# Kernel optimization log

Hardware: AMD Instinct MI355X
Metric: run time of the kernel (lower is better)

Reference implementation:

```python
import jax, jax.numpy as jnp
import numpy as np

B, S, D_IN, D_OUT = 8, 4096, 512, 64

def setup_inputs() -> dict:
    key = jax.random.key(0)
    k1, k2, k3, k4 = jax.random.split(key, 4)
    scale = 1.0 / np.sqrt(D_IN)
    return {
        "x": jax.random.normal(k1, (B, S, D_IN), dtype=jnp.float32),
        "W_Q": jax.random.normal(k2, (D_IN, D_OUT), dtype=jnp.float32) * scale,
        "W_K": jax.random.normal(k3, (D_IN, D_OUT), dtype=jnp.float32) * scale,
        "W_V": jax.random.normal(k4, (D_IN, D_OUT), dtype=jnp.float32) * scale,
    }

def reference(x, W_Q, W_K, W_V):
    # q,k,v: [B,S,D_OUT]
    q = jnp.einsum("bsd,de->bse", x, W_Q)
    k = jnp.einsum("bsd,de->bse", x, W_K)
    v = jnp.einsum("bsd,de->bse", x, W_V)
    d_out = k.shape[-1]
    # scores: [B,S,S], causal mask (upper triangle -> -inf)
    scores = jnp.einsum("bqe,bke->bqk", q, k)
    s = q.shape[1]
    causal = jnp.tril(jnp.ones((s, s), dtype=bool))
    scores = jnp.where(causal[None, :, :], scores, -jnp.inf)
    attn = jax.nn.softmax(scores / jnp.sqrt(jnp.asarray(d_out, scores.dtype)), axis=-1)
    # dropout p=0.0 (eval) -> identity
    return jnp.einsum("bqk,bke->bqe", attn, v)
```

## Files before the change

kernel.cpp:

```cpp
#include <hip/hip_runtime.h>
#include <hip/hip_bf16.h>

#define B_    8
#define S_    4096
#define DIN   512
#define DOUT  64
#define NROWS (B_ * S_)

typedef __attribute__((ext_vector_type(8)))  short bf16x8;
typedef __attribute__((ext_vector_type(4)))  float f32x4;
typedef __attribute__((ext_vector_type(16))) float f32x16;
typedef __attribute__((ext_vector_type(2)))  unsigned int u32x2;
typedef __attribute__((ext_vector_type(2)))  int i32x2;

typedef const __attribute__((address_space(1))) unsigned int GUI;
typedef __attribute__((address_space(3))) unsigned int LUI;

__device__ __forceinline__ unsigned short f32_to_bf16(float f) {
    union { float f; unsigned int u; } c; c.f = f;
    unsigned int r = (c.u + 0x7FFFu + ((c.u >> 16) & 1u)) >> 16;
    return (unsigned short)r;
}
__device__ __forceinline__ float bf16_to_f32(unsigned short us) {
    union { unsigned int u; float f; } c; c.u = (unsigned int)us << 16;
    return c.f;
}

__device__ __forceinline__ float fast_exp2(float x) {
#if __has_builtin(__builtin_amdgcn_exp2f)
    return __builtin_amdgcn_exp2f(x);
#else
    return exp2f(x);
#endif
}

__device__ __forceinline__ float sum_xor32(float v) {
    i32x2 r = __builtin_amdgcn_permlane32_swap(__float_as_int(v), __float_as_int(v),
                                               false, false);
    return __int_as_float(r.x) + __int_as_float(r.y);
}

#define LDS_READS_DONE_FENCE() do {                                   \
    asm volatile("s_waitcnt lgkmcnt(0)" ::: "memory");                \
    __builtin_amdgcn_sched_barrier(0);                                \
} while (0)

__device__ __forceinline__ int pidx_of(int tp, int j) {
    if (tp < 16) return tp - 8;
    if (tp < 24) return 8 + (tp - 16) * 2 + (j - 1);
    return 24 + (tp - 24) * 3 + (j - 1);
}

#define PART_STRIDE 16896

__global__ void wt_convert(const float* __restrict__ WQ,
                           const float* __restrict__ WK,
                           const float* __restrict__ WV,
                           unsigned short* __restrict__ Wt2) {
    int idx = blockIdx.x * 256 + threadIdx.x;
    if (idx >= 3 * 512 * 16) return;
    int p   = idx / 8192;
    int rem = idx - p * 8192;
    int k   = rem >> 4;
    int n0  = (rem & 15) * 4;
    const float* W = (p == 0) ? WQ : ((p == 1) ? WK : WV);
    float4 v = *(const float4*)(W + k * 64 + n0);
    const int ks = k >> 5, kl = k & 31;
    float vv[4] = {v.x, v.y, v.z, v.w};
#pragma unroll
    for (int r = 0; r < 4; ++r) {
        int n = n0 + r;
        Wt2[(size_t)((ks * 12 + p * 4 + (n >> 4)) * 512) + (n & 15) * 32 + kl] =
            f32_to_bf16(vv[r]);
    }
}

__global__ __launch_bounds__(256) void qkv_proj(const float* __restrict__ x,
                                                const unsigned short* __restrict__ Wt2,
                                                unsigned short* __restrict__ QKV) {
    __shared__ alignas(16) float          xtile[2][1024];
    __shared__ alignas(16) unsigned short btile[2][6144];

    const int tid  = threadIdx.x;
    const int lane = tid & 63;
    const int wq   = tid >> 6;
    const int c15  = lane & 15;
    const int g    = lane >> 4;
    const float* xblk = x + (size_t)blockIdx.x * 32 * DIN;

    const int rw     = (wq & 1) * 16 + c15;
    const int nfbase = (wq >> 1) * 6;

    const int xrow = wq * 8 + (lane >> 3);
    const int xsl  = (lane & 7) ^ (xrow & 7);

    auto stage = [&](int slot, int ks) {
        __builtin_amdgcn_global_load_lds((GUI*)(xblk + ks * 32 + xrow * DIN + xsl * 4),
                                         (LUI*)((char*)&xtile[slot][0] + wq * 1024), 16, 0, 0);
        const unsigned short* Bs = Wt2 + (size_t)ks * 6144;
#pragma unroll
        for (int j = 0; j < 3; ++j)
            __builtin_amdgcn_global_load_lds((GUI*)(Bs + (j * 256 + tid) * 8),
                                             (LUI*)((char*)&btile[slot][0] + j * 4096 + wq * 1024),
                                             16, 0, 0);
    };
    stage(0, 0);
    stage(1, 1);

    f32x4 acc[6] = {};

    int cur = 0;
    for (int ks = 0; ks < 16; ++ks) {
        asm volatile("s_waitcnt vmcnt(4)" ::: "memory");
        asm volatile("s_barrier" ::: "memory");

        const char* xb = (const char*)&xtile[cur][0] + rw * 128;
        f32x4 a0 = *(const f32x4*)(xb + (((2 * g)     ^ (rw & 7)) << 4));
        f32x4 a1 = *(const f32x4*)(xb + (((2 * g + 1) ^ (rw & 7)) << 4));
        union { unsigned w[4]; bf16x8 v; } af;
        asm("v_cvt_pk_bf16_f32 %0, %1, %2" : "=v"(af.w[0]) : "v"(a0[0]), "v"(a0[1]));
        asm("v_cvt_pk_bf16_f32 %0, %1, %2" : "=v"(af.w[1]) : "v"(a0[2]), "v"(a0[3]));
        asm("v_cvt_pk_bf16_f32 %0, %1, %2" : "=v"(af.w[2]) : "v"(a1[0]), "v"(a1[1]));
        asm("v_cvt_pk_bf16_f32 %0, %1, %2" : "=v"(af.w[3]) : "v"(a1[2]), "v"(a1[3]));

        const char* bb = (const char*)&btile[cur][0] + c15 * 64 + g * 16;
#pragma unroll
        for (int n = 0; n < 6; ++n) {
            bf16x8 bf = *(const bf16x8*)(bb + (nfbase + n) * 1024);
            acc[n] = __builtin_amdgcn_mfma_f32_16x16x32_bf16(af.v, bf, acc[n], 0, 0, 0);
        }

        LDS_READS_DONE_FENCE();
        asm volatile("s_barrier" ::: "memory");
        {
            int tn = ks + 2; if (tn > 15) tn = 15;
            stage(cur, tn);
        }
        cur ^= 1;
    }
    asm volatile("s_waitcnt vmcnt(0)" ::: "memory");

    const int orow0 = blockIdx.x * 32 + (wq & 1) * 16 + g * 4;
#pragma unroll
    for (int n = 0; n < 6; ++n) {
        const int nfg  = nfbase + n;
        const int p    = nfg >> 2;
        const int ncol = (nfg & 3) * 16 + c15;
        if (p < 2) {
            unsigned short* outp = QKV + (size_t)p * NROWS * DOUT;
            const float sc = (p == 0) ? 0.125f * 1.44269504089f : 1.0f;
#pragma unroll
            for (int r = 0; r < 4; ++r)
                outp[(size_t)(orow0 + r) * DOUT + ncol] = f32_to_bf16(acc[n][r] * sc);
        } else {
            const int bb2  = orow0 >> 12;
            const int srow = orow0 & 4095;
            union { unsigned short s[4]; u32x2 d; } pk;
#pragma unroll
            for (int r = 0; r < 4; ++r) pk.s[r] = f32_to_bf16(acc[n][r]);
            *(u32x2*)(QKV + (size_t)2 * NROWS * DOUT +
                      ((size_t)bb2 * DOUT + ncol) * S_ + srow) = pk.d;
        }
    }
}

__global__ __launch_bounds__(512) void qk_norms(const unsigned short* __restrict__ QKV,
                                                float* __restrict__ qn,
                                                float* __restrict__ ktm) {
    __shared__ float lds[64];
    const int bid  = blockIdx.x;
    const bool isK = bid >= 512;
    const int blk  = isK ? bid - 512 : bid;
    const int tid  = threadIdx.x;
    const int rowl = tid >> 3;
    const int part = tid & 7;
    const size_t row = (size_t)blk * 64 + rowl;

    const unsigned short* src = QKV + (isK ? (size_t)NROWS * DOUT : 0) +
                                row * DOUT + part * 8;
    bf16x8 v = *(const bf16x8*)src;
    float s = 0.f;
#pragma unroll
    for (int i2 = 0; i2 < 8; ++i2) {
        float f = bf16_to_f32((unsigned short)v[i2]);
        s += f * f;
    }
    s += __shfl_xor(s, 1, 64);
    s += __shfl_xor(s, 2, 64);
    s += __shfl_xor(s, 4, 64);

    if (!isK) {
        if (part == 0) qn[row] = sqrtf(s);
    } else {
        if (part == 0) lds[rowl] = s;
        __syncthreads();
        if (tid < 64) {
            float m = lds[tid];
#pragma unroll
            for (int st = 32; st >= 1; st >>= 1)
                m = fmaxf(m, __shfl_xor(m, st, 64));
            if (tid == 0) ktm[blk] = sqrtf(m);
        }
    }
}

__global__ void kpref(const float* __restrict__ ktm, float* __restrict__ pm) {
    const int b = threadIdx.x;
    if (b >= 8) return;
    float m = 0.f;
    for (int t = 0; t < 64; ++t) {
        m = fmaxf(m, ktm[b * 64 + t]);
        pm[b * 64 + t] = m;
    }
}

__global__ __launch_bounds__(256) void attn_fwd(const unsigned short* __restrict__ QKV,
                                                const float* __restrict__ qn,
                                                const float* __restrict__ pm,
                                                float* __restrict__ out,
                                                char* __restrict__ part1,
                                                float* __restrict__ ml0) {
    __shared__ alignas(16) unsigned short k_lds[2][4096];
    __shared__ alignas(16) unsigned short v_lds[2][4096];

    const int bid = blockIdx.x;
    const int b   = bid & 7;
    const int i   = 79 - (bid >> 3);
    int tp, j;
    if      (i < 8)  { tp = i;                   j = 0; }
    else if (i < 24) { tp = 8 + ((i - 8) >> 1);  j = (i - 8) & 1; }
    else if (i < 48) { tp = 16 + (i - 24) / 3;   j = (i - 24) % 3; }
    else             { tp = 24 + ((i - 48) >> 2); j = (i - 48) & 3; }
    const int qb       = tp * 128;
    const int tile_lo  = 16 * j;
    const int tile_hi  = min(16 * j + 15, 2 * tp + 1);
    const int tile_cnt = tile_hi - tile_lo + 1;

    const int tid  = threadIdx.x;
    const int lane = tid & 63;
    const int wq   = tid >> 6;
    const int q31  = lane & 31;
    const int h    = lane >> 5;
    const int swz  = q31 & 7;
    const int rb0  = q31 * 128;

    const unsigned short* Qg  = QKV + (size_t)b * S_ * DOUT;
    const unsigned short* Kg  = QKV + (size_t)NROWS * DOUT + (size_t)b * S_ * DOUT;
    const unsigned short* VTg = QKV + (size_t)2 * NROWS * DOUT + (size_t)b * DOUT * S_;

    const int qrow = qb + wq * 32 + q31;
    const unsigned short* Qr = Qg + (size_t)qrow * DOUT + 8 * h;
    bf16x8 qf[4];
#pragma unroll
    for (int s = 0; s < 4; ++s) qf[s] = *(const bf16x8*)(Qr + 16 * s);

    const float M_r = qn[(size_t)b * S_ + qrow] * pm[b * 64 + (qrow >> 6)];
    asm volatile("s_waitcnt vmcnt(0)" ::: "memory");

    const int i0 = wq * 128 + lane;
    const int i1 = i0 + 64;
    const int r0 = i0 >> 3, s0g = (i0 & 7) ^ (r0 & 7);
    const int r1 = i1 >> 3, s1g = (i1 & 7) ^ (r1 & 7);

    auto stage = [&](int slot, int tg) {
        const unsigned short* Kt = Kg + (size_t)tg * 64 * DOUT;
        const unsigned short* Vt = VTg + tg * 64;
        char* kbase = (char*)&k_lds[slot][0] + wq * 2048;
        char* vbase = (char*)&v_lds[slot][0] + wq * 2048;
        __builtin_amdgcn_global_load_lds((GUI*)(Kt + r0 * DOUT + s0g * 8), (LUI*)kbase, 16, 0, 0);
        __builtin_amdgcn_global_load_lds((GUI*)(Kt + r1 * DOUT + s1g * 8), (LUI*)(kbase + 1024), 16, 0, 0);
        __builtin_amdgcn_global_load_lds((GUI*)(Vt + (size_t)r0 * S_ + s0g * 8), (LUI*)vbase, 16, 0, 0);
        __builtin_amdgcn_global_load_lds((GUI*)(Vt + (size_t)r1 * S_ + s1g * 8), (LUI*)(vbase + 1024), 16, 0, 0);
    };

    stage(0, tile_lo);
    stage(1, tile_lo + 1);

    f32x16 oacc0 = {}, oacc1 = {};
    float l_r = 0.f;

    int cur = 0;
    for (int itl = 0; itl < tile_cnt; ++itl) {
        const int tg = tile_lo + itl;
        asm volatile("s_waitcnt vmcnt(4)" ::: "memory");
        asm volatile("s_barrier" ::: "memory");

        const char* kb_ = (const char*)&k_lds[cur][0];
        const char* vb_ = (const char*)&v_lds[cur][0];

        f32x16 sA = {}, sB = {};
#pragma unroll
        for (int s = 0; s < 4; ++s) {
            const int sl = ((2 * s + h) ^ swz) << 4;
            bf16x8 ka  = *(const bf16x8*)(kb_ + rb0 + sl);
            bf16x8 kb2 = *(const bf16x8*)(kb_ + rb0 + 4096 + sl);
            sA = __builtin_amdgcn_mfma_f32_32x32x16_bf16(ka,  qf[s], sA, 0, 0, 0);
            sB = __builtin_amdgcn_mfma_f32_32x32x16_bf16(kb2, qf[s], sB, 0, 0, 0);
        }

        if (tg >= 2 * tp) {
#pragma unroll
            for (int r2 = 0; r2 < 16; ++r2) {
                const int kvg = 64 * tg + (r2 & 3) + 8 * (r2 >> 2) + 4 * h;
                if (kvg      > qrow) sA[r2] = -1.0e30f;
                if (kvg + 32 > qrow) sB[r2] = -1.0e30f;
            }
        }

        float t0 = 0.f, t1 = 0.f, t2 = 0.f, t3 = 0.f;
#pragma unroll
        for (int k2 = 0; k2 < 16; ++k2) {
            sA[k2] = fast_exp2(sA[k2] - M_r);
            sB[k2] = fast_exp2(sB[k2] - M_r);
        }
#pragma unroll
        for (int k2 = 0; k2 < 4; ++k2) {
            t0 += sA[k2];      t1 += sA[k2 + 4];
            t0 += sA[k2 + 8];  t1 += sA[k2 + 12];
            t2 += sB[k2];      t3 += sB[k2 + 4];
            t2 += sB[k2 + 8];  t3 += sB[k2 + 12];
        }
        l_r += (t0 + t1) + (t2 + t3);

#define STEP_PV(u, Pv) do {                                                        \
        const int e0 = 2 * ((u) & 1);                                              \
        unsigned pa, pb2, pc, pd;                                                  \
        asm("v_cvt_pk_bf16_f32 %0, %1, %2" : "=v"(pa)  : "v"(Pv[4*e0+0]), "v"(Pv[4*e0+1])); \
        asm("v_cvt_pk_bf16_f32 %0, %1, %2" : "=v"(pb2) : "v"(Pv[4*e0+2]), "v"(Pv[4*e0+3])); \
        asm("v_cvt_pk_bf16_f32 %0, %1, %2" : "=v"(pc)  : "v"(Pv[4*e0+4]), "v"(Pv[4*e0+5])); \
        asm("v_cvt_pk_bf16_f32 %0, %1, %2" : "=v"(pd)  : "v"(Pv[4*e0+6]), "v"(Pv[4*e0+7])); \
        i32x2 ra = __builtin_amdgcn_permlane32_swap((int)pa,  (int)pc, false, false); \
        i32x2 rb = __builtin_amdgcn_permlane32_swap((int)pb2, (int)pd, false, false); \
        union { unsigned w[4]; bf16x8 v; } pw;                                     \
        pw.w[0] = (unsigned)ra.x; pw.w[1] = (unsigned)rb.x;                        \
        pw.w[2] = (unsigned)ra.y; pw.w[3] = (unsigned)rb.y;                        \
        const int slv = ((2 * (u) + h) ^ swz) << 4;                                \
        bf16x8 vfa = *(const bf16x8*)(vb_ + rb0 + slv);                            \
        bf16x8 vfb = *(const bf16x8*)(vb_ + rb0 + 4096 + slv);                     \
        oacc0 = __builtin_amdgcn_mfma_f32_32x32x16_bf16(vfa, pw.v, oacc0, 0, 0, 0);\
        oacc1 = __builtin_amdgcn_mfma_f32_32x32x16_bf16(vfb, pw.v, oacc1, 0, 0, 0);\
    } while (0)

        STEP_PV(0, sA); STEP_PV(1, sA); STEP_PV(2, sB); STEP_PV(3, sB);
#undef STEP_PV

        LDS_READS_DONE_FENCE();
        asm volatile("s_barrier" ::: "memory");
        {
            int tn = itl + 2; if (tn >= tile_cnt) tn = tile_cnt - 1;
            stage(cur, tile_lo + tn);
        }
        cur ^= 1;
    }

    asm volatile("s_waitcnt vmcnt(0)" ::: "memory");

    l_r = sum_xor32(l_r);

    const int ql = wq * 32 + q31;
    if (j == 0 && tp < 8) {
        const float linv = 1.0f / l_r;
        float* op = out + (size_t)b * S_ * DOUT + (size_t)qrow * DOUT;
#pragma unroll
        for (int e = 0; e < 4; ++e) {
            f32x4 v0 = { oacc0[4*e+0]*linv, oacc0[4*e+1]*linv, oacc0[4*e+2]*linv, oacc0[4*e+3]*linv };
            f32x4 v1 = { oacc1[4*e+0]*linv, oacc1[4*e+1]*linv, oacc1[4*e+2]*linv, oacc1[4*e+3]*linv };
            *(f32x4*)(op + 8*e + 4*h)      = v0;
            *(f32x4*)(op + 32 + 8*e + 4*h) = v1;
        }
    } else if (j == 0) {
        float* op = out + (size_t)b * S_ * DOUT + (size_t)qrow * DOUT;
#pragma unroll
        for (int e = 0; e < 4; ++e) {
            f32x4 v0 = { oacc0[4*e+0], oacc0[4*e+1], oacc0[4*e+2], oacc0[4*e+3] };
            f32x4 v1 = { oacc1[4*e+0], oacc1[4*e+1], oacc1[4*e+2], oacc1[4*e+3] };
            *(f32x4*)(op + 8*e + 4*h)      = v0;
            *(f32x4*)(op + 32 + 8*e + 4*h) = v1;
        }
        if (h == 0) ml0[(size_t)(b * 24 + (tp - 8)) * 128 + ql] = l_r;
    } else {
        char* pb_ = part1 + (size_t)(b * 48 + pidx_of(tp, j)) * PART_STRIDE;
        if (h == 0) ((float*)pb_)[ql] = l_r;
        unsigned short* ob = (unsigned short*)(pb_ + 512);
#pragma unroll
        for (int e = 0; e < 4; ++e) {
            union { unsigned short s[4]; u32x2 d; } k0, k1;
#pragma unroll
            for (int c = 0; c < 4; ++c) { k0.s[c] = f32_to_bf16(oacc0[4*e+c]);
                                          k1.s[c] = f32_to_bf16(oacc1[4*e+c]); }
            *(u32x2*)(ob + (size_t)ql * 64 + 8*e + 4*h)      = k0.d;
            *(u32x2*)(ob + (size_t)ql * 64 + 32 + 8*e + 4*h) = k1.d;
        }
    }
}

template<int NC>
__device__ __forceinline__ void reduce_body(int b, int tp, int q, int d,
                                            float* __restrict__ out,
                                            const char* __restrict__ part1,
                                            const float* __restrict__ ml0) {
    float* otile = out + ((size_t)b * S_ + (size_t)tp * 128) * 64;
    float L = ml0[(size_t)(b * 24 + (tp - 8)) * 128 + q];
    float O = otile[(size_t)q * 64 + d];
#pragma unroll
    for (int jj = 0; jj < NC - 1; ++jj) {
        const char* pb = part1 + (size_t)(b * 48 + pidx_of(tp, jj + 1)) * PART_STRIDE;
        L += ((const float*)pb)[q];
        O += bf16_to_f32(((const unsigned short*)(pb + 512))[(size_t)q * 64 + d]);
    }
    otile[(size_t)q * 64 + d] = O / L;
}

__global__ __launch_bounds__(256) void attn_reduce(float* __restrict__ out,
                                                   const char* __restrict__ part1,
                                                   const float* __restrict__ ml0) {
    const int bid = blockIdx.x;
    const int sub = bid & 31;
    const int tz  = (bid >> 5) % 24;
    const int b   = bid / (32 * 24);
    const int tp  = tz + 8;
    const int q   = sub * 4 + (threadIdx.x >> 6);
    const int d   = threadIdx.x & 63;

    if (tp < 16)      reduce_body<2>(b, tp, q, d, out, part1, ml0);
    else if (tp < 24) reduce_body<3>(b, tp, q, d, out, part1, ml0);
    else              reduce_body<4>(b, tp, q, d, out, part1, ml0);
}

extern "C" void kernel_launch(void* const* d_in, const int* in_sizes, int n_in,
                              void* d_out, int out_size, void* d_ws, size_t ws_size,
                              hipStream_t stream) {
    const float* x  = (const float*)d_in[0];
    const float* WQ = (const float*)d_in[1];
    const float* WK = (const float*)d_in[2];
    const float* WV = (const float*)d_in[3];

    unsigned short* Wt2   = (unsigned short*)d_ws;
    unsigned short* QKV   = Wt2 + 192 * 512;
    char*           part1 = (char*)d_ws + 12779520;
    float*          ml0   = (float*)((char*)d_ws + 19267584);
    float*          qn    = (float*)((char*)d_ws + 19365888);
    float*          ktm   = (float*)((char*)d_ws + 19496960);
    float*          pmb   = (float*)((char*)d_ws + 19499008);
    float* out = (float*)d_out;

    wt_convert<<<96, 256, 0, stream>>>(WQ, WK, WV, Wt2);
    qkv_proj<<<1024, 256, 0, stream>>>(x, Wt2, QKV);
    qk_norms<<<1024, 512, 0, stream>>>(QKV, qn, ktm);
    kpref<<<1, 64, 0, stream>>>(ktm, pmb);
    attn_fwd<<<640, 256, 0, stream>>>(QKV, qn, pmb, out, part1, ml0);
    attn_reduce<<<6144, 256, 0, stream>>>(out, part1, ml0);
}
```

Baseline: 78.24 us.

## Load K/V fragments directly from global memory instead of LDS double buffering

Removes the shared-memory double-buffered K/V staging, with its barriers and async global-to-LDS loads. Each wave now loads its K and V MFMA fragments straight from global memory into registers every tile, and s_setprio is raised around the MFMA sections. This drops LDS traffic and block-wide synchronisation and frees LDS for occupancy. In exchange, the four waves each fetch the same K/V tile redundantly, the loads are no longer prefetched ahead of use, and latency may be exposed because of that.

```diff
diff --git a/kernel.cpp b/kernel.cpp
--- a/kernel.cpp
+++ b/kernel.cpp
@@ -220,9 +220,6 @@
                                                 float* __restrict__ out,
                                                 char* __restrict__ part1,
                                                 float* __restrict__ ml0) {
-    __shared__ alignas(16) unsigned short k_lds[2][4096];
-    __shared__ alignas(16) unsigned short v_lds[2][4096];
-
     const int bid = blockIdx.x;
     const int b   = bid & 7;
     const int i   = 79 - (bid >> 3);
@@ -241,8 +238,6 @@
     const int wq   = tid >> 6;
     const int q31  = lane & 31;
     const int h    = lane >> 5;
-    const int swz  = q31 & 7;
-    const int rb0  = q31 * 128;
 
     const unsigned short* Qg  = QKV + (size_t)b * S_ * DOUT;
     const unsigned short* Kg  = QKV + (size_t)NROWS * DOUT + (size_t)b * S_ * DOUT;
@@ -255,48 +250,40 @@
     for (int s = 0; s < 4; ++s) qf[s] = *(const bf16x8*)(Qr + 16 * s);
 
     const float M_r = qn[(size_t)b * S_ + qrow] * pm[b * 64 + (qrow >> 6)];
-    asm volatile("s_waitcnt vmcnt(0)" ::: "memory");
-
-    const int i0 = wq * 128 + lane;
-    const int i1 = i0 + 64;
-    const int r0 = i0 >> 3, s0g = (i0 & 7) ^ (r0 & 7);
-    const int r1 = i1 >> 3, s1g = (i1 & 7) ^ (r1 & 7);
-
-    auto stage = [&](int slot, int tg) {
-        const unsigned short* Kt = Kg + (size_t)tg * 64 * DOUT;
-        const unsigned short* Vt = VTg + tg * 64;
-        char* kbase = (char*)&k_lds[slot][0] + wq * 2048;
-        char* vbase = (char*)&v_lds[slot][0] + wq * 2048;
-        __builtin_amdgcn_global_load_lds((GUI*)(Kt + r0 * DOUT + s0g * 8), (LUI*)kbase, 16, 0, 0);
-        __builtin_amdgcn_global_load_lds((GUI*)(Kt + r1 * DOUT + s1g * 8), (LUI*)(kbase + 1024), 16, 0, 0);
-        __builtin_amdgcn_global_load_lds((GUI*)(Vt + (size_t)r0 * S_ + s0g * 8), (LUI*)vbase, 16, 0, 0);
-        __builtin_amdgcn_global_load_lds((GUI*)(Vt + (size_t)r1 * S_ + s1g * 8), (LUI*)(vbase + 1024), 16, 0, 0);
-    };
-
-    stage(0, tile_lo);
-    stage(1, tile_lo + 1);
+
+    const unsigned short* Krow0 = Kg + (size_t)q31 * DOUT + 8 * h;
+    const unsigned short* Krow1 = Kg + (size_t)(q31 + 32) * DOUT + 8 * h;
+    const unsigned short* Vrow0 = VTg + (size_t)q31 * S_ + 8 * h;
+    const unsigned short* Vrow1 = VTg + (size_t)(q31 + 32) * S_ + 8 * h;
 
     f32x16 oacc0 = {}, oacc1 = {};
     float l_r = 0.f;
 
-    int cur = 0;
     for (int itl = 0; itl < tile_cnt; ++itl) {
-        const int tg = tile_lo + itl;
-        asm volatile("s_waitcnt vmcnt(4)" ::: "memory");
-        asm volatile("s_barrier" ::: "memory");
-
-        const char* kb_ = (const char*)&k_lds[cur][0];
-        const char* vb_ = (const char*)&v_lds[cur][0];
+        const int tg  = tile_lo + itl;
+        const size_t koff = (size_t)tg * 64 * DOUT;
+        const int    voff = tg * 64;
+
+        bf16x8 ka[4], kb2[4], va[4], vb2[4];
+#pragma unroll
+        for (int s = 0; s < 4; ++s) {
+            ka[s]  = *(const bf16x8*)(Krow0 + koff + 16 * s);
+            kb2[s] = *(const bf16x8*)(Krow1 + koff + 16 * s);
+        }
+#pragma unroll
+        for (int u = 0; u < 4; ++u) {
+            va[u]  = *(const bf16x8*)(Vrow0 + voff + 16 * u);
+            vb2[u] = *(const bf16x8*)(Vrow1 + voff + 16 * u);
+        }
 
         f32x16 sA = {}, sB = {};
+        __builtin_amdgcn_s_setprio(1);
 #pragma unroll
         for (int s = 0; s < 4; ++s) {
-            const int sl = ((2 * s + h) ^ swz) << 4;
-            bf16x8 ka  = *(const bf16x8*)(kb_ + rb0 + sl);
-            bf16x8 kb2 = *(const bf16x8*)(kb_ + rb0 + 4096 + sl);
-            sA = __builtin_amdgcn_mfma_f32_32x32x16_bf16(ka,  qf[s], sA, 0, 0, 0);
-            sB = __builtin_amdgcn_mfma_f32_32x32x16_bf16(kb2, qf[s], sB, 0, 0, 0);
-        }
+            sA = __builtin_amdgcn_mfma_f32_32x32x16_bf16(ka[s],  qf[s], sA, 0, 0, 0);
+            sB = __builtin_amdgcn_mfma_f32_32x32x16_bf16(kb2[s], qf[s], sB, 0, 0, 0);
+        }
+        __builtin_amdgcn_s_setprio(0);
 
         if (tg >= 2 * tp) {
 #pragma unroll
@@ -334,26 +321,15 @@
         union { unsigned w[4]; bf16x8 v; } pw;                                     \
         pw.w[0] = (unsigned)ra.x; pw.w[1] = (unsigned)rb.x;                        \
         pw.w[2] = (unsigned)ra.y; pw.w[3] = (unsigned)rb.y;                        \
-        const int slv = ((2 * (u) + h) ^ swz) << 4;                                \
-        bf16x8 vfa = *(const bf16x8*)(vb_ + rb0 + slv);                            \
-        bf16x8 vfb = *(const bf16x8*)(vb_ + rb0 + 4096 + slv);                     \
-        oacc0 = __builtin_amdgcn_mfma_f32_32x32x16_bf16(vfa, pw.v, oacc0, 0, 0, 0);\
-        oacc1 = __builtin_amdgcn_mfma_f32_32x32x16_bf16(vfb, pw.v, oacc1, 0, 0, 0);\
+        oacc0 = __builtin_amdgcn_mfma_f32_32x32x16_bf16(va[u],  pw.v, oacc0, 0, 0, 0);\
+        oacc1 = __builtin_amdgcn_mfma_f32_32x32x16_bf16(vb2[u], pw.v, oacc1, 0, 0, 0);\
     } while (0)
 
+        __builtin_amdgcn_s_setprio(1);
         STEP_PV(0, sA); STEP_PV(1, sA); STEP_PV(2, sB); STEP_PV(3, sB);
+        __builtin_amdgcn_s_setprio(0);
 #undef STEP_PV
-
-        LDS_READS_DONE_FENCE();
-        asm volatile("s_barrier" ::: "memory");
-        {
-            int tn = itl + 2; if (tn >= tile_cnt) tn = tile_cnt - 1;
-            stage(cur, tile_lo + tn);
-        }
-        cur ^= 1;
-    }
-
-    asm volatile("s_waitcnt vmcnt(0)" ::: "memory");
+    }
 
     l_r = sum_xor32(l_r);
 
```

Measured after the change: 126.0 us. +61.0%, slower.

## Split attention blocks into two 64-query halves and add MFMA priority hints

Applied to the files above, without the earlier changes.

The attention kernel now launches twice as many 128-thread blocks, each covering 64 query rows instead of 128, with K/V staging loops restructured so each thread issues 8 async loads per tile. The intent is better occupancy and load balance across CUs for the causal, split-KV schedule. The cost is that every K/V tile is now loaded by two blocks instead of one. s_setprio is raised around the MFMA sections to favour matrix issue. The kpref prefix-max is also parallelised across 8 blocks and 64 threads, each computing its own prefix.

```diff
diff --git a/kernel.cpp b/kernel.cpp
--- a/kernel.cpp
+++ b/kernel.cpp
@@ -205,16 +205,14 @@
 }
 
 __global__ void kpref(const float* __restrict__ ktm, float* __restrict__ pm) {
-    const int b = threadIdx.x;
-    if (b >= 8) return;
+    const int b = blockIdx.x;
+    const int t = threadIdx.x;
     float m = 0.f;
-    for (int t = 0; t < 64; ++t) {
-        m = fmaxf(m, ktm[b * 64 + t]);
-        pm[b * 64 + t] = m;
-    }
-}
-
-__global__ __launch_bounds__(256) void attn_fwd(const unsigned short* __restrict__ QKV,
+    for (int u = 0; u <= t; ++u) m = fmaxf(m, ktm[b * 64 + u]);
+    pm[b * 64 + t] = m;
+}
+
+__global__ __launch_bounds__(128) void attn_fwd(const unsigned short* __restrict__ QKV,
                                                 const float* __restrict__ qn,
                                                 const float* __restrict__ pm,
                                                 float* __restrict__ out,
@@ -223,15 +221,16 @@
     __shared__ alignas(16) unsigned short k_lds[2][4096];
     __shared__ alignas(16) unsigned short v_lds[2][4096];
 
-    const int bid = blockIdx.x;
-    const int b   = bid & 7;
-    const int i   = 79 - (bid >> 3);
+    const int bid  = blockIdx.x;
+    const int b    = bid & 7;
+    const int idx  = bid >> 3;
+    const int half = idx & 1;
+    const int i    = 79 - (idx >> 1);
     int tp, j;
     if      (i < 8)  { tp = i;                   j = 0; }
     else if (i < 24) { tp = 8 + ((i - 8) >> 1);  j = (i - 8) & 1; }
     else if (i < 48) { tp = 16 + (i - 24) / 3;   j = (i - 24) % 3; }
     else             { tp = 24 + ((i - 48) >> 2); j = (i - 48) & 3; }
-    const int qb       = tp * 128;
     const int tile_lo  = 16 * j;
     const int tile_hi  = min(16 * j + 15, 2 * tp + 1);
     const int tile_cnt = tile_hi - tile_lo + 1;
@@ -248,7 +247,8 @@
     const unsigned short* Kg  = QKV + (size_t)NROWS * DOUT + (size_t)b * S_ * DOUT;
     const unsigned short* VTg = QKV + (size_t)2 * NROWS * DOUT + (size_t)b * DOUT * S_;
 
-    const int qrow = qb + wq * 32 + q31;
+    const int ql128 = half * 64 + wq * 32 + q31;
+    const int qrow  = tp * 128 + ql128;
     const unsigned short* Qr = Qg + (size_t)qrow * DOUT + 8 * h;
     bf16x8 qf[4];
 #pragma unroll
@@ -256,21 +256,24 @@
 
     const float M_r = qn[(size_t)b * S_ + qrow] * pm[b * 64 + (qrow >> 6)];
     asm volatile("s_waitcnt vmcnt(0)" ::: "memory");
-
-    const int i0 = wq * 128 + lane;
-    const int i1 = i0 + 64;
-    const int r0 = i0 >> 3, s0g = (i0 & 7) ^ (r0 & 7);
-    const int r1 = i1 >> 3, s1g = (i1 & 7) ^ (r1 & 7);
 
     auto stage = [&](int slot, int tg) {
         const unsigned short* Kt = Kg + (size_t)tg * 64 * DOUT;
         const unsigned short* Vt = VTg + tg * 64;
-        char* kbase = (char*)&k_lds[slot][0] + wq * 2048;
-        char* vbase = (char*)&v_lds[slot][0] + wq * 2048;
-        __builtin_amdgcn_global_load_lds((GUI*)(Kt + r0 * DOUT + s0g * 8), (LUI*)kbase, 16, 0, 0);
-        __builtin_amdgcn_global_load_lds((GUI*)(Kt + r1 * DOUT + s1g * 8), (LUI*)(kbase + 1024), 16, 0, 0);
-        __builtin_amdgcn_global_load_lds((GUI*)(Vt + (size_t)r0 * S_ + s0g * 8), (LUI*)vbase, 16, 0, 0);
-        __builtin_amdgcn_global_load_lds((GUI*)(Vt + (size_t)r1 * S_ + s1g * 8), (LUI*)(vbase + 1024), 16, 0, 0);
+#pragma unroll
+        for (int r = 0; r < 4; ++r) {
+            const int i2  = r * 128 + tid;
+            const int row = i2 >> 3, sl = (i2 & 7) ^ (row & 7);
+            __builtin_amdgcn_global_load_lds((GUI*)(Kt + row * DOUT + sl * 8),
+                (LUI*)((char*)&k_lds[slot][0] + r * 2048 + wq * 1024), 16, 0, 0);
+        }
+#pragma unroll
+        for (int r = 0; r < 4; ++r) {
+            const int i2  = r * 128 + tid;
+            const int row = i2 >> 3, sl = (i2 & 7) ^ (row & 7);
+            __builtin_amdgcn_global_load_lds((GUI*)(Vt + (size_t)row * S_ + sl * 8),
+                (LUI*)((char*)&v_lds[slot][0] + r * 2048 + wq * 1024), 16, 0, 0);
+        }
     };
 
     stage(0, tile_lo);
@@ -282,13 +285,14 @@
     int cur = 0;
     for (int itl = 0; itl < tile_cnt; ++itl) {
         const int tg = tile_lo + itl;
-        asm volatile("s_waitcnt vmcnt(4)" ::: "memory");
+        asm volatile("s_waitcnt vmcnt(8)" ::: "memory");
         asm volatile("s_barrier" ::: "memory");
 
         const char* kb_ = (const char*)&k_lds[cur][0];
         const char* vb_ = (const char*)&v_lds[cur][0];
 
         f32x16 sA = {}, sB = {};
+        __builtin_amdgcn_s_setprio(1);
 #pragma unroll
         for (int s = 0; s < 4; ++s) {
             const int sl = ((2 * s + h) ^ swz) << 4;
@@ -297,6 +301,7 @@
             sA = __builtin_amdgcn_mfma_f32_32x32x16_bf16(ka,  qf[s], sA, 0, 0, 0);
             sB = __builtin_amdgcn_mfma_f32_32x32x16_bf16(kb2, qf[s], sB, 0, 0, 0);
         }
+        __builtin_amdgcn_s_setprio(0);
 
         if (tg >= 2 * tp) {
 #pragma unroll
@@ -341,7 +346,9 @@
         oacc1 = __builtin_amdgcn_mfma_f32_32x32x16_bf16(vfb, pw.v, oacc1, 0, 0, 0);\
     } while (0)
 
+        __builtin_amdgcn_s_setprio(1);
         STEP_PV(0, sA); STEP_PV(1, sA); STEP_PV(2, sB); STEP_PV(3, sB);
+        __builtin_amdgcn_s_setprio(0);
 #undef STEP_PV
 
         LDS_READS_DONE_FENCE();
@@ -357,7 +364,6 @@
 
     l_r = sum_xor32(l_r);
 
-    const int ql = wq * 32 + q31;
     if (j == 0 && tp < 8) {
         const float linv = 1.0f / l_r;
         float* op = out + (size_t)b * S_ * DOUT + (size_t)qrow * DOUT;
@@ -377,10 +383,10 @@
             *(f32x4*)(op + 8*e + 4*h)      = v0;
             *(f32x4*)(op + 32 + 8*e + 4*h) = v1;
         }
-        if (h == 0) ml0[(size_t)(b * 24 + (tp - 8)) * 128 + ql] = l_r;
+        if (h == 0) ml0[(size_t)(b * 24 + (tp - 8)) * 128 + ql128] = l_r;
     } else {
         char* pb_ = part1 + (size_t)(b * 48 + pidx_of(tp, j)) * PART_STRIDE;
-        if (h == 0) ((float*)pb_)[ql] = l_r;
+        if (h == 0) ((float*)pb_)[ql128] = l_r;
         unsigned short* ob = (unsigned short*)(pb_ + 512);
 #pragma unroll
         for (int e = 0; e < 4; ++e) {
@@ -388,8 +394,8 @@
 #pragma unroll
             for (int c = 0; c < 4; ++c) { k0.s[c] = f32_to_bf16(oacc0[4*e+c]);
                                           k1.s[c] = f32_to_bf16(oacc1[4*e+c]); }
-            *(u32x2*)(ob + (size_t)ql * 64 + 8*e + 4*h)      = k0.d;
-            *(u32x2*)(ob + (size_t)ql * 64 + 32 + 8*e + 4*h) = k1.d;
+            *(u32x2*)(ob + (size_t)ql128 * 64 + 8*e + 4*h)      = k0.d;
+            *(u32x2*)(ob + (size_t)ql128 * 64 + 32 + 8*e + 4*h) = k1.d;
         }
     }
 }
@@ -447,7 +453,7 @@
     wt_convert<<<96, 256, 0, stream>>>(WQ, WK, WV, Wt2);
     qkv_proj<<<1024, 256, 0, stream>>>(x, Wt2, QKV);
     qk_norms<<<1024, 512, 0, stream>>>(QKV, qn, ktm);
-    kpref<<<1, 64, 0, stream>>>(ktm, pmb);
-    attn_fwd<<<640, 256, 0, stream>>>(QKV, qn, pmb, out, part1, ml0);
+    kpref<<<8, 64, 0, stream>>>(ktm, pmb);
+    attn_fwd<<<1280, 128, 0, stream>>>(QKV, qn, pmb, out, part1, ml0);
     attn_reduce<<<6144, 256, 0, stream>>>(out, part1, ml0);
 }
```

New measurement: 88.42 us. 13.0% more time.
